# Performance work log

Hardware: AMD Instinct MI355X
Metric: run time of the kernel (lower is better)

## Reference

```python
import jax, jax.numpy as jnp
import numpy as np

B, N, DIM, HEADS = 8, 512, 512, 16
MAX_DIST, NG = 128, 32
RBF_STOP = 20.0
EPS = 1e-5


def _ln(x, g, b):
    m = jnp.mean(x, axis=-1, keepdims=True)
    v = jnp.mean((x - m) ** 2, axis=-1, keepdims=True)
    return (x - m) * jax.lax.rsqrt(v + EPS) * g + b


def setup_inputs() -> dict:
    key = jax.random.key(0)
    ks = jax.random.split(key, 12)
    d = DIM
    s = 0.02
    return {
        "x": jax.random.normal(ks[0], (B * N, d), jnp.float32),
        "dist_matrix": jax.random.randint(ks[1], (B, N, N), 0, MAX_DIST, jnp.int32),
        "dist_3d": jax.random.uniform(ks[2], (B, N, N), jnp.float32) * RBF_STOP,
        "norm1_g": jnp.ones((d,), jnp.float32),
        "norm1_b": jnp.zeros((d,), jnp.float32),
        "in_proj_w": jax.random.normal(ks[3], (3 * d, d), jnp.float32) * s,
        "in_proj_b": jnp.zeros((3 * d,), jnp.float32),
        "out_proj_w": jax.random.normal(ks[4], (d, d), jnp.float32) * s,
        "out_proj_b": jnp.zeros((d,), jnp.float32),
        "dist_emb": jax.random.normal(ks[5], (MAX_DIST, HEADS), jnp.float32) * s,
        "rbf_w": jax.random.normal(ks[6], (HEADS, NG), jnp.float32) * s,
        "rbf_b": jnp.zeros((HEADS,), jnp.float32),
        "norm2_g": jnp.ones((d,), jnp.float32),
        "norm2_b": jnp.zeros((d,), jnp.float32),
        "ffn_w1": jax.random.normal(ks[7], (4 * d, d), jnp.float32) * s,
        "ffn_b1": jnp.zeros((4 * d,), jnp.float32),
        "ffn_w2": jax.random.normal(ks[8], (d, 4 * d), jnp.float32) * s,
        "ffn_b2": jnp.zeros((d,), jnp.float32),
        "batch": jnp.repeat(jnp.arange(B, dtype=jnp.int32), N),
    }


def reference(x, dist_matrix, dist_3d, norm1_g, norm1_b, in_proj_w, in_proj_b,
              out_proj_w, out_proj_b, dist_emb, rbf_w, rbf_b, norm2_g, norm2_b,
              ffn_w1, ffn_b1, ffn_w2, ffn_b2, batch):
    b, n = dist_matrix.shape[0], dist_matrix.shape[1]
    d = x.shape[-1]
    dh = d // HEADS
    # equal-size graphs -> to_dense_batch is a reshape, mask all-true
    xd = x.reshape(b, n, d)

    # additive attention bias: shortest-path-distance embedding + RBF projection
    dc = jnp.clip(dist_matrix, 0, MAX_DIST - 1)
    bias_spd = dist_emb[dc]                                  # [b, n, n, H]
    offset = jnp.linspace(0.0, RBF_STOP, NG, dtype=jnp.float32)
    coeff = -0.5 / (RBF_STOP / (NG - 1)) ** 2
    rbf = jnp.exp(coeff * (dist_3d[..., None] - offset) ** 2)  # [b, n, n, NG]
    bias_3d = rbf @ rbf_w.T + rbf_b                          # [b, n, n, H]
    bias = jnp.transpose(bias_spd + bias_3d, (0, 3, 1, 2))   # [b, H, n, n]

    # multi-head attention (pre-norm residual, as in source)
    h = _ln(xd, norm1_g, norm1_b)
    qkv = h @ in_proj_w.T + in_proj_b
    q, k, v = jnp.split(qkv, 3, axis=-1)
    q = q.reshape(b, n, HEADS, dh).transpose(0, 2, 1, 3)
    k = k.reshape(b, n, HEADS, dh).transpose(0, 2, 1, 3)
    v = v.reshape(b, n, HEADS, dh).transpose(0, 2, 1, 3)
    scores = jnp.einsum('bhqd,bhkd->bhqk', q, k) / jnp.sqrt(jnp.float32(dh)) + bias
    attn = jax.nn.softmax(scores, axis=-1)
    ctx = jnp.einsum('bhqk,bhkd->bhqd', attn, v)
    ctx = ctx.transpose(0, 2, 1, 3).reshape(b, n, d)
    attn_out = ctx @ out_proj_w.T + out_proj_b
    h = h + attn_out

    # FFN (dropout inactive at eval)
    h2 = _ln(h, norm2_g, norm2_b)
    ff = jax.nn.gelu(h2 @ ffn_w1.T + ffn_b1, approximate=False) @ ffn_w2.T + ffn_b2
    h = h + ff
    return h.reshape(b * n, d)
```

## Files before the change

kernel.cpp:

```cpp
#include <hip/hip_runtime.h>
#include <hip/hip_bf16.h>
#include <math.h>

#define BB 8
#define NN 512
#define DD 512
#define NH 16
#define DH 32
#define TD 1536
#define NG 32
#define MAXD 128

typedef __attribute__((ext_vector_type(8))) short bf16x8;
typedef __attribute__((ext_vector_type(4))) float f32x4;
typedef __attribute__((ext_vector_type(2))) unsigned int u32x2;
typedef __attribute__((ext_vector_type(4))) unsigned int u32x4;

__device__ inline short f2bf(float x) {
    __hip_bfloat16 h = __float2bfloat16(x);
    return *reinterpret_cast<short*>(&h);
}
__device__ inline float bf2f(short x) {
    union { unsigned u; float f; } c;
    c.u = ((unsigned)(unsigned short)x) << 16;
    return c.f;
}
__device__ inline unsigned cvt_pk_bf16(float lo, float hi) {
    unsigned r;
    asm("v_cvt_pk_bf16_f32 %0, %1, %2" : "=v"(r) : "v"(lo), "v"(hi));
    return r;
}
__device__ inline float exp2fast(float x) {
    float r;
    asm("v_exp_f32 %0, %1" : "=v"(r) : "v"(x));
    return r;
}

__device__ inline void gld_lds16(const void* g, void* l) {
    __builtin_amdgcn_global_load_lds(
        (const __attribute__((address_space(1))) unsigned int*)g,
        (__attribute__((address_space(3))) unsigned int*)l, 16, 0, 0);
}

__global__ __launch_bounds__(256) void prep(
    const float* __restrict__ x, const float* __restrict__ n1g,
    const float* __restrict__ n1b, short* __restrict__ h_bf,
    const float* __restrict__ s0, const float* __restrict__ s1,
    const float* __restrict__ s2, const float* __restrict__ s3,
    short* __restrict__ d0, short* __restrict__ d1,
    short* __restrict__ d2, short* __restrict__ d3,
    const float* __restrict__ rbfw, const float* __restrict__ rbfb,
    short* __restrict__ Tg,
    int n0, int n1, int n2, int n3) {
    const int tid = threadIdx.x;
    if (blockIdx.x < 4096) {
        const int row = blockIdx.x;
        const int wave = tid >> 6, lane = tid & 63;
        const float* xr = x + (size_t)row * DD;
        const float2 v01 = *(const float2*)(xr + 2 * tid);
        float s = v01.x + v01.y, q = v01.x * v01.x + v01.y * v01.y;
#pragma unroll
        for (int m = 1; m < 64; m <<= 1) { s += __shfl_xor(s, m); q += __shfl_xor(q, m); }
        __shared__ float ps[8];
        if (lane == 0) { ps[wave] = s; ps[wave + 4] = q; }
        __syncthreads();
        s = ps[0] + ps[1] + ps[2] + ps[3];
        q = ps[4] + ps[5] + ps[6] + ps[7];
        const float mean = s * (1.0f / DD);
        const float var  = q * (1.0f / DD) - mean * mean;
        const float rs   = rsqrtf(var + 1e-5f);
        const float2 g2 = *(const float2*)(n1g + 2 * tid);
        const float2 b2 = *(const float2*)(n1b + 2 * tid);
        const float o0 = (v01.x - mean) * rs * g2.x + b2.x;
        const float o1 = (v01.y - mean) * rs * g2.y + b2.y;
        *(unsigned*)&h_bf[(size_t)row * DD + 2 * tid] = cvt_pk_bf16(o0, o1);
        return;
    }
    const int bx = blockIdx.x - 4096;
    const int y = bx >> 9, xb = bx & 511;
    if (y == 4) {
        if (xb != 0) return;
        const float STEP  = 20.0f / 31.0f;
        const float COEFF = -0.5f / (STEP * STEP);
        for (int idx = tid; idx < 194 * 16; idx += 256) {
            const int i = idx >> 4, h = idx & 15;
            const float xx = fminf((float)i, 192.0f) * (20.0f / 192.0f);
            float acc = rbfb[h];
#pragma unroll
            for (int g = 0; g < NG; g++) {
                const float t = xx - (float)g * STEP;
                acc += __expf(COEFF * t * t) * rbfw[h * NG + g];
            }
            Tg[idx] = f2bf(acc * 1.44269504088896f);
        }
        return;
    }
    const float* s; short* d; int n;
    switch (y) {
        case 0: s = s0; d = d0; n = n0; break;
        case 1: s = s1; d = d1; n = n1; break;
        case 2: s = s2; d = d2; n = n2; break;
        default: s = s3; d = d3; n = n3; break;
    }
    const int i = (xb * 256 + tid) * 8;
    if (i >= n) return;
    const float4 a = *(const float4*)(s + i);
    const float4 b = *(const float4*)(s + i + 4);
    u32x4 o;
    o[0] = cvt_pk_bf16(a.x, a.y);
    o[1] = cvt_pk_bf16(a.z, a.w);
    o[2] = cvt_pk_bf16(b.x, b.y);
    o[3] = cvt_pk_bf16(b.z, b.w);
    *(u32x4*)(d + i) = o;
}

template <int TM, bool GELU, int RESMODE, bool OUTBF>
__global__ __launch_bounds__(256) void gemm_bf16(
    const short* __restrict__ A, const short* __restrict__ Bw,
    const float* __restrict__ bias, const void* __restrict__ res,
    void* __restrict__ Cout, int M, int Nout, int K) {
    const int MI = (TM >= 32) ? TM / 32 : 1;
    const int bm = blockIdx.y * TM;
    const int bn = blockIdx.x * 128;
    const int tid  = threadIdx.x;
    const int wave = tid >> 6;
    const int lane = tid & 63;
    const int l16  = lane & 15;
    const int quad = lane >> 4;
    const int wr = (wave >> 1) * (TM / 2);
    const int wc = (wave & 1) * 64;

    __shared__ short As[2][TM * 32];
    __shared__ short Bs[2][128 * 32];

    f32x4 acc[MI][4];
#pragma unroll
    for (int i = 0; i < MI; i++)
#pragma unroll
        for (int j = 0; j < 4; j++) acc[i][j] = (f32x4){0.f, 0.f, 0.f, 0.f};

    auto stage = [&](int buf, int k0) {
        const short* Ab = A + (size_t)bm * K + k0;
        const short* Bb = Bw + (size_t)bn * K + k0;
        if (TM >= 64) {
#pragma unroll
            for (int j = 0; j < TM / 64; j++) {
                const int idx = j * 256 + tid;
                gld_lds16(Ab + (size_t)(idx >> 2) * K + (idx & 3) * 8,
                          &As[buf][(size_t)(j * 256 + wave * 64) * 8]);
            }
        } else {
            if (tid < 128)
                gld_lds16(Ab + (size_t)(tid >> 2) * K + (tid & 3) * 8,
                          &As[buf][(size_t)(wave * 64) * 8]);
        }
#pragma unroll
        for (int j = 0; j < 2; j++) {
            const int idx = j * 256 + tid;
            gld_lds16(Bb + (size_t)(idx >> 2) * K + (idx & 3) * 8,
                      &Bs[buf][(size_t)(j * 256 + wave * 64) * 8]);
        }
    };
    auto compute = [&](int buf) {
        bf16x8 af[MI], bfr[4];
#pragma unroll
        for (int i = 0; i < MI; i++)
            af[i] = *(const bf16x8*)&As[buf][(wr + i * 16 + l16) * 32 + quad * 8];
#pragma unroll
        for (int j = 0; j < 4; j++)
            bfr[j] = *(const bf16x8*)&Bs[buf][(wc + j * 16 + l16) * 32 + quad * 8];
#pragma unroll
        for (int i = 0; i < MI; i++)
#pragma unroll
            for (int j = 0; j < 4; j++)
                acc[i][j] = __builtin_amdgcn_mfma_f32_16x16x32_bf16(bfr[j], af[i], acc[i][j], 0, 0, 0);
    };

    stage(0, 0);
    __syncthreads();
    int cur = 0;
    for (int k0 = 32; k0 < K; k0 += 32) {
        stage(cur ^ 1, k0);
        compute(cur);
        __syncthreads();
        cur ^= 1;
    }
    compute(cur);

#pragma unroll
    for (int i = 0; i < MI; i++) {
        const int row = bm + wr + i * 16 + l16;
#pragma unroll
        for (int j = 0; j < 4; j++) {
            const int col = bn + wc + j * 16 + quad * 4;
            const float4 b4 = *(const float4*)&bias[col];
            float v[4] = {acc[i][j][0] + b4.x, acc[i][j][1] + b4.y,
                          acc[i][j][2] + b4.z, acc[i][j][3] + b4.w};
            if (GELU) {
#pragma unroll
                for (int r = 0; r < 4; r++)
                    v[r] = 0.5f * v[r] * (1.0f + erff(v[r] * 0.70710678118654752f));
            }
            if (RESMODE == 1) {
                const float4 r4 = *(const float4*)&((const float*)res)[(size_t)row * Nout + col];
                v[0] += r4.x; v[1] += r4.y; v[2] += r4.z; v[3] += r4.w;
            }
            if (RESMODE == 2) {
                const short4 r4 = *(const short4*)&((const short*)res)[(size_t)row * Nout + col];
                v[0] += bf2f(r4.x); v[1] += bf2f(r4.y); v[2] += bf2f(r4.z); v[3] += bf2f(r4.w);
            }
            if (OUTBF) {
                u32x2 o;
                o[0] = cvt_pk_bf16(v[0], v[1]);
                o[1] = cvt_pk_bf16(v[2], v[3]);
                *(u32x2*)&((short*)Cout)[(size_t)row * Nout + col] = o;
            } else {
                *(float4*)&((float*)Cout)[(size_t)row * Nout + col] =
                    (float4){v[0], v[1], v[2], v[3]};
            }
        }
    }
}

__global__ __launch_bounds__(512, 4) void attn_fused(
    const short* __restrict__ qkv,
    const int* __restrict__ dist,
    const float* __restrict__ dist3d,
    const float* __restrict__ demb,
    const short* __restrict__ Tg,
    const short* __restrict__ wo,
    const float* __restrict__ bo,
    const short* __restrict__ hb,
    const float* __restrict__ g2v,
    const float* __restrict__ b2v,
    float* __restrict__ hres,
    short* __restrict__ h2) {
    const int blk  = blockIdx.x;
    const int b    = blk & 7;
    const int q0   = (blk >> 3) * 16;
    const int tid  = threadIdx.x;
    const int wave = tid >> 6;
    const int lane = tid & 63;
    const int l16  = lane & 15;
    const int quad = lane >> 4;
    const int hh0  = wave * 2;

    __shared__ short Vc[NH * 1024];
    __shared__ short Pb[16 * 512];
    __shared__ short Tt[194 * 18];
    __shared__ short Db[128 * 18];
    __shared__ unsigned short Pk[512 * 16];
    __shared__ float St[2][16][8];

    for (int i = tid; i < 194 * 16; i += 512) Tt[(i >> 4) * 18 + (i & 15)] = Tg[i];
    for (int i = tid; i < 128 * 16; i += 512)
        Db[(i >> 4) * 18 + (i & 15)] = f2bf(demb[i] * 1.44269504088896f);
    {
        const size_t rb = ((size_t)(b * NN) + q0) * NN;
#pragma unroll
        for (int q = 0; q < 16; q++) {
            const size_t off = rb + (size_t)q * NN + tid;
            int dc = dist[off];
            dc = min(max(dc, 0), MAXD - 1);
            int ii = (int)(dist3d[off] * 9.6f + 0.5f);
            ii = min(ii, 192);
            Pk[tid * 16 + q] = (unsigned short)(dc | (ii << 8));
        }
    }

    const float scale = 0.17677669529663687f * 1.44269504088896f;
    bf16x8 qf[2];
#pragma unroll
    for (int h = 0; h < 2; h++)
        qf[h] = *(const bf16x8*)(qkv + (size_t)(b * NN + q0 + l16) * TD + (hh0 + h) * DH + quad * 8);

    f32x4 O[2][2];
    float lsum[2][4];
#pragma unroll
    for (int h = 0; h < 2; h++) {
#pragma unroll
        for (int tt = 0; tt < 2; tt++) O[h][tt] = (f32x4){0.f, 0.f, 0.f, 0.f};
#pragma unroll
        for (int r = 0; r < 4; r++) lsum[h][r] = 0.f;
    }

    __syncthreads();

    const int sk = lane >> 2;
    const int sc = lane & 3;

    auto stageV = [&](int c) {
        const size_t rowb = (size_t)(b * NN + c * 32 + sk) * TD + 2 * DD + sc * 8;
#pragma unroll
        for (int h = 0; h < 2; h++) {
            short* dst = &Vc[(hh0 + h) * 1024];
            gld_lds16(qkv + rowb + (hh0 + h) * DH, dst);
            gld_lds16(qkv + rowb + (size_t)16 * TD + (hh0 + h) * DH, dst + 512);
        }
    };
    auto loadK = [&](int c, bf16x8 (*kd)[2]) {
#pragma unroll
        for (int h = 0; h < 2; h++) {
            const short* base =
                qkv + (size_t)(b * NN + c * 32 + l16) * TD + DD + (hh0 + h) * DH + quad * 8;
            kd[h][0] = *(const bf16x8*)base;
            kd[h][1] = *(const bf16x8*)(base + 16 * TD);
        }
    };

    bf16x8 kf[2][2], kfn[2][2];
    stageV(0);
    loadK(0, kf);

    for (int c = 0; c < 16; c++) {
        asm volatile("" ::: "memory");
        __builtin_amdgcn_s_waitcnt(0x0F70);
        asm volatile("" ::: "memory");

        u32x2 vraw[2][4];
#pragma unroll
        for (int h = 0; h < 2; h++) {
            const unsigned va =
                (unsigned)(uintptr_t)&Vc[(hh0 + h) * 1024 + quad * 128 + l16];
            asm volatile("ds_read_b64_tr_b16 %0, %1 offset:0"    : "=v"(vraw[h][0]) : "v"(va));
            asm volatile("ds_read_b64_tr_b16 %0, %1 offset:128"  : "=v"(vraw[h][1]) : "v"(va));
            asm volatile("ds_read_b64_tr_b16 %0, %1 offset:1024" : "=v"(vraw[h][2]) : "v"(va));
            asm volatile("ds_read_b64_tr_b16 %0, %1 offset:1152" : "=v"(vraw[h][3]) : "v"(va));
        }
        asm volatile("s_waitcnt lgkmcnt(0)" ::: "memory");
        __builtin_amdgcn_sched_barrier(0);

        if (c + 1 < 16) {
            stageV(c + 1);
            loadK(c + 1, kfn);
        }

#pragma unroll
        for (int half = 0; half < 2; half++) {
            const ushort4 pk4 =
                *(const ushort4*)&Pk[(unsigned)((c * 32 + half * 16 + l16) * 16 + quad * 4)];
            const unsigned short pe[4] = {pk4.x, pk4.y, pk4.z, pk4.w};
            float bb[2][4];
#pragma unroll
            for (int r = 0; r < 4; r++) {
                const unsigned u  = pe[r];
                const unsigned dc = u & 0xFFu;
                const unsigned ii = u >> 8;
                const unsigned du = *(const unsigned*)&Db[dc * 18 + hh0];
                const unsigned tu = *(const unsigned*)&Tt[ii * 18 + hh0];
                union { unsigned x; float f; } a0, a1, b0, b1;
                a0.x = du << 16; a1.x = du & 0xFFFF0000u;
                b0.x = tu << 16; b1.x = tu & 0xFFFF0000u;
                bb[0][r] = a0.f + b0.f;
                bb[1][r] = a1.f + b1.f;
            }
#pragma unroll
            for (int h = 0; h < 2; h++) {
                f32x4 s = __builtin_amdgcn_mfma_f32_16x16x32_bf16(
                    qf[h], kf[h][half], (f32x4){0.f, 0.f, 0.f, 0.f}, 0, 0, 0);
                float pv[4];
#pragma unroll
                for (int r = 0; r < 4; r++) {
                    float sv = s[r] * scale + bb[h][r];
                    sv = fminf(sv, 28.853901f);
                    pv[r] = exp2fast(sv);
                    lsum[h][r] += pv[r];
                }
                u32x2 w;
                w[0] = cvt_pk_bf16(pv[0], pv[1]);
                w[1] = cvt_pk_bf16(pv[2], pv[3]);
                *(u32x2*)&Pb[(wave * 2 + h) * 512 + (half * 16 + l16) * 16 + quad * 4] = w;
            }
        }

        asm volatile("" ::: "memory");
        asm volatile("s_waitcnt lgkmcnt(0)" ::: "memory");
        __builtin_amdgcn_sched_barrier(0);

        u32x2 praw[2][2];
#pragma unroll
        for (int h = 0; h < 2; h++) {
            const unsigned pa =
                (unsigned)(uintptr_t)&Pb[(wave * 2 + h) * 512 + quad * 64 + l16];
            asm volatile("ds_read_b64_tr_b16 %0, %1 offset:0"   : "=v"(praw[h][0]) : "v"(pa));
            asm volatile("ds_read_b64_tr_b16 %0, %1 offset:512" : "=v"(praw[h][1]) : "v"(pa));
        }
        asm volatile("s_waitcnt lgkmcnt(0)" ::: "memory");
        __builtin_amdgcn_sched_barrier(0);

        __builtin_amdgcn_s_setprio(1);
#pragma unroll
        for (int h = 0; h < 2; h++) {
            union { u32x4 u; bf16x8 s; } pf, v0, v1;
            pf.u = (u32x4){praw[h][0][0], praw[h][0][1], praw[h][1][0], praw[h][1][1]};
#pragma unroll
            for (int r = 0; r < 4; r++) {
                v0.u[r] = __builtin_amdgcn_perm(vraw[h][r][1], vraw[h][r][0], 0x05040100u);
                v1.u[r] = __builtin_amdgcn_perm(vraw[h][r][1], vraw[h][r][0], 0x07060302u);
            }
            O[h][0] = __builtin_amdgcn_mfma_f32_16x16x32_bf16(pf.s, v0.s, O[h][0], 0, 0, 0);
            O[h][1] = __builtin_amdgcn_mfma_f32_16x16x32_bf16(pf.s, v1.s, O[h][1], 0, 0, 0);
        }
        __builtin_amdgcn_s_setprio(0);

#pragma unroll
        for (int h = 0; h < 2; h++) { kf[h][0] = kfn[h][0]; kf[h][1] = kfn[h][1]; }
    }

#pragma unroll
    for (int h = 0; h < 2; h++) {
#pragma unroll
        for (int m = 1; m < 16; m <<= 1)
#pragma unroll
            for (int r = 0; r < 4; r++) lsum[h][r] += __shfl_xor(lsum[h][r], m);
        float rl[4];
#pragma unroll
        for (int r = 0; r < 4; r++) rl[r] = 1.0f / lsum[h][r];
#pragma unroll
        for (int tt = 0; tt < 2; tt++) {
            const int col = (hh0 + h) * DH + tt * 16 + l16;
            u32x2 w;
            w[0] = cvt_pk_bf16(O[h][tt][0] * rl[0], O[h][tt][1] * rl[1]);
            w[1] = cvt_pk_bf16(O[h][tt][2] * rl[2], O[h][tt][3] * rl[3]);
            *(u32x2*)&Pb[col * 16 + quad * 4] = w;
        }
    }
    __syncthreads();

    const int rowg = b * NN + q0;
    const int wcol = wave * 64;
    short hbr[4][4];
#pragma unroll
    for (int j = 0; j < 4; j++)
#pragma unroll
        for (int r = 0; r < 4; r++)
            hbr[j][r] = hb[((size_t)rowg + quad * 4 + r) * DD + wcol + j * 16 + l16];

    f32x4 a2[4];
#pragma unroll
    for (int j = 0; j < 4; j++) a2[j] = (f32x4){0.f, 0.f, 0.f, 0.f};
    u32x2 blo[2][4], bhi[2][4];
#pragma unroll
    for (int j = 0; j < 4; j++) {
        const short* wb = wo + (size_t)(wcol + j * 16 + l16) * DD + quad * 4;
        blo[0][j] = *(const u32x2*)wb;
        bhi[0][j] = *(const u32x2*)(wb + 16);
    }
#pragma unroll
    for (int kk = 0; kk < 16; kk++) {
        const int k0 = kk * 32;
        u32x2 p0, p1;
        const unsigned pa = (unsigned)(uintptr_t)&Pb[k0 * 16 + quad * 64 + l16];
        asm volatile("ds_read_b64_tr_b16 %0, %1 offset:0"   : "=v"(p0) : "v"(pa));
        asm volatile("ds_read_b64_tr_b16 %0, %1 offset:512" : "=v"(p1) : "v"(pa));
        if (kk + 1 < 16) {
#pragma unroll
            for (int j = 0; j < 4; j++) {
                const short* wb =
                    wo + (size_t)(wcol + j * 16 + l16) * DD + (k0 + 32) + quad * 4;
                blo[(kk + 1) & 1][j] = *(const u32x2*)wb;
                bhi[(kk + 1) & 1][j] = *(const u32x2*)(wb + 16);
            }
        }
        asm volatile("s_waitcnt lgkmcnt(0)" ::: "memory");
        __builtin_amdgcn_sched_barrier(0);
        union { u32x4 u; bf16x8 s; } af;
        af.u = (u32x4){p0[0], p0[1], p1[0], p1[1]};
#pragma unroll
        for (int j = 0; j < 4; j++) {
            union { u32x4 u; bf16x8 s; } bw;
            bw.u = (u32x4){blo[kk & 1][j][0], blo[kk & 1][j][1],
                           bhi[kk & 1][j][0], bhi[kk & 1][j][1]};
            a2[j] = __builtin_amdgcn_mfma_f32_16x16x32_bf16(af.s, bw.s, a2[j], 0, 0, 0);
        }
    }

    float vv[4][4];
    float sp[4] = {0.f, 0.f, 0.f, 0.f}, qp[4] = {0.f, 0.f, 0.f, 0.f};
#pragma unroll
    for (int j = 0; j < 4; j++) {
        const int col = wcol + j * 16 + l16;
        const float bc = bo[col];
#pragma unroll
        for (int r = 0; r < 4; r++) {
            const size_t row = (size_t)rowg + quad * 4 + r;
            const float v = a2[j][r] + bc + bf2f(hbr[j][r]);
            hres[row * DD + col] = v;
            vv[j][r] = v;
            sp[r] += v; qp[r] += v * v;
        }
    }
#pragma unroll
    for (int m = 1; m < 16; m <<= 1)
#pragma unroll
        for (int r = 0; r < 4; r++) {
            sp[r] += __shfl_xor(sp[r], m);
            qp[r] += __shfl_xor(qp[r], m);
        }
    if (l16 == 0) {
#pragma unroll
        for (int r = 0; r < 4; r++) {
            St[0][quad * 4 + r][wave] = sp[r];
            St[1][quad * 4 + r][wave] = qp[r];
        }
    }
    __syncthreads();
    float mean[4], rsd[4];
#pragma unroll
    for (int r = 0; r < 4; r++) {
        const int rr = quad * 4 + r;
        float s = 0.f, q = 0.f;
#pragma unroll
        for (int w = 0; w < 8; w++) { s += St[0][rr][w]; q += St[1][rr][w]; }
        mean[r] = s * (1.0f / DD);
        rsd[r]  = rsqrtf(q * (1.0f / DD) - mean[r] * mean[r] + 1e-5f);
    }
#pragma unroll
    for (int j = 0; j < 4; j++) {
        const int col = wcol + j * 16 + l16;
        const float gc = g2v[col], bc2 = b2v[col];
#pragma unroll
        for (int r = 0; r < 4; r++) {
            const size_t row = (size_t)rowg + quad * 4 + r;
            h2[row * DD + col] = f2bf((vv[j][r] - mean[r]) * rsd[r] * gc + bc2);
        }
    }
}

extern "C" void kernel_launch(void* const* d_in, const int* in_sizes, int n_in,
                              void* d_out, int out_size, void* d_ws, size_t ws_size,
                              hipStream_t stream) {
    const float* x      = (const float*)d_in[0];
    const int*   dist   = (const int*)d_in[1];
    const float* dist3d = (const float*)d_in[2];
    const float* n1g    = (const float*)d_in[3];
    const float* n1b    = (const float*)d_in[4];
    const float* win    = (const float*)d_in[5];
    const float* bin    = (const float*)d_in[6];
    const float* wo     = (const float*)d_in[7];
    const float* bo     = (const float*)d_in[8];
    const float* demb   = (const float*)d_in[9];
    const float* rbfw   = (const float*)d_in[10];
    const float* rbfb   = (const float*)d_in[11];
    const float* n2g    = (const float*)d_in[12];
    const float* n2b    = (const float*)d_in[13];
    const float* w1     = (const float*)d_in[14];
    const float* b1     = (const float*)d_in[15];
    const float* w2     = (const float*)d_in[16];
    const float* b2     = (const float*)d_in[17];

    char* p = (char*)d_ws;
    short* h_bf   = (short*)p; p += (size_t)4096 * 512 * 2;
    short* qkv_bf = (short*)p; p += (size_t)4096 * 1536 * 2;
    float* hres   = (float*)p; p += (size_t)4096 * 512 * 4;
    short* h2_bf  = (short*)p; p += (size_t)4096 * 512 * 2;
    short* win_bf = (short*)p; p += (size_t)1536 * 512 * 2;
    short* wo_bf  = (short*)p; p += (size_t)512 * 512 * 2;
    short* w1_bf  = (short*)p; p += (size_t)2048 * 512 * 2;
    short* w2_bf  = (short*)p; p += (size_t)512 * 2048 * 2;
    short* Tg     = (short*)p; p += (size_t)8192;
    short* mid_bf = (short*)p; p += (size_t)4096 * 2048 * 2;

    const int M = BB * NN;

    prep<<<4096 + 2560, 256, 0, stream>>>(
        x, n1g, n1b, h_bf,
        win, wo, w1, w2, win_bf, wo_bf, w1_bf, w2_bf, rbfw, rbfb, Tg,
        1536 * 512, 512 * 512, 2048 * 512, 512 * 2048);
    gemm_bf16<128, false, 0, true><<<dim3(12, 32), 256, 0, stream>>>(
        h_bf, win_bf, bin, nullptr, qkv_bf, M, TD, DD);
    attn_fused<<<256, 512, 0, stream>>>(
        qkv_bf, dist, dist3d, demb, Tg, wo_bf, bo, h_bf, n2g, n2b, hres, h2_bf);
    gemm_bf16<128, true, 0, true><<<dim3(16, 32), 256, 0, stream>>>(
        h2_bf, w1_bf, b1, nullptr, mid_bf, M, 2048, DD);
    gemm_bf16<32, false, 1, false><<<dim3(4, 128), 256, 0, stream>>>(
        mid_bf, w2_bf, b2, hres, (float*)d_out, M, DD, 2048);
}
```

Baseline: 260.2 us.

## Use one wave per head in fused attention with 1024-thread blocks

The fused attention kernel goes from 8 waves each handling two heads to 16 waves each handling one head, doubling the block size to 1024 threads. The out-projection/LayerNorm epilogue is re-split so each wave owns 32 output columns instead of 64, and the row statistics reduce over 16 waves. The aim is more latency hiding and less per-wave serial work, since the grid has only 256 blocks. In exchange the bias lookup now does separate 16-bit loads per head, and 1024-thread blocks limit how many blocks fit per CU and raise per-block sync cost.

```diff
diff --git a/kernel.cpp b/kernel.cpp
--- a/kernel.cpp
+++ b/kernel.cpp
@@ -222,7 +222,7 @@
     }
 }
 
-__global__ __launch_bounds__(512, 4) void attn_fused(
+__global__ __launch_bounds__(1024, 4) void attn_fused(
     const short* __restrict__ qkv,
     const int* __restrict__ dist,
     const float* __restrict__ dist3d,
@@ -243,46 +243,41 @@
     const int lane = tid & 63;
     const int l16  = lane & 15;
     const int quad = lane >> 4;
-    const int hh0  = wave * 2;
+    const int hh   = wave;
 
     __shared__ short Vc[NH * 1024];
     __shared__ short Pb[16 * 512];
     __shared__ short Tt[194 * 18];
     __shared__ short Db[128 * 18];
     __shared__ unsigned short Pk[512 * 16];
-    __shared__ float St[2][16][8];
-
-    for (int i = tid; i < 194 * 16; i += 512) Tt[(i >> 4) * 18 + (i & 15)] = Tg[i];
-    for (int i = tid; i < 128 * 16; i += 512)
+    __shared__ float St[2][16][16];
+
+    for (int i = tid; i < 194 * 16; i += 1024) Tt[(i >> 4) * 18 + (i & 15)] = Tg[i];
+    for (int i = tid; i < 128 * 16; i += 1024)
         Db[(i >> 4) * 18 + (i & 15)] = f2bf(demb[i] * 1.44269504088896f);
     {
         const size_t rb = ((size_t)(b * NN) + q0) * NN;
-#pragma unroll
-        for (int q = 0; q < 16; q++) {
-            const size_t off = rb + (size_t)q * NN + tid;
+        for (int i = tid; i < 16 * 512; i += 1024) {
+            const int q = i >> 9, k = i & 511;
+            const size_t off = rb + (size_t)q * NN + k;
             int dc = dist[off];
             dc = min(max(dc, 0), MAXD - 1);
             int ii = (int)(dist3d[off] * 9.6f + 0.5f);
             ii = min(ii, 192);
-            Pk[tid * 16 + q] = (unsigned short)(dc | (ii << 8));
+            Pk[k * 16 + q] = (unsigned short)(dc | (ii << 8));
         }
     }
 
     const float scale = 0.17677669529663687f * 1.44269504088896f;
-    bf16x8 qf[2];
-#pragma unroll
-    for (int h = 0; h < 2; h++)
-        qf[h] = *(const bf16x8*)(qkv + (size_t)(b * NN + q0 + l16) * TD + (hh0 + h) * DH + quad * 8);
-
-    f32x4 O[2][2];
-    float lsum[2][4];
-#pragma unroll
-    for (int h = 0; h < 2; h++) {
-#pragma unroll
-        for (int tt = 0; tt < 2; tt++) O[h][tt] = (f32x4){0.f, 0.f, 0.f, 0.f};
-#pragma unroll
-        for (int r = 0; r < 4; r++) lsum[h][r] = 0.f;
-    }
+    const bf16x8 qf =
+        *(const bf16x8*)(qkv + (size_t)(b * NN + q0 + l16) * TD + hh * DH + quad * 8);
+
+    f32x4 O[2];
+    float lsum[4];
+#pragma unroll
+    for (int tt = 0; tt < 2; tt++) O[tt] = (f32x4){0.f, 0.f, 0.f, 0.f};
+#pragma unroll
+    for (int r = 0; r < 4; r++) lsum[r] = 0.f;
 
     __syncthreads();
 
@@ -291,24 +286,18 @@
 
     auto stageV = [&](int c) {
         const size_t rowb = (size_t)(b * NN + c * 32 + sk) * TD + 2 * DD + sc * 8;
-#pragma unroll
-        for (int h = 0; h < 2; h++) {
-            short* dst = &Vc[(hh0 + h) * 1024];
-            gld_lds16(qkv + rowb + (hh0 + h) * DH, dst);
-            gld_lds16(qkv + rowb + (size_t)16 * TD + (hh0 + h) * DH, dst + 512);
-        }
+        short* dst = &Vc[hh * 1024];
+        gld_lds16(qkv + rowb + hh * DH, dst);
+        gld_lds16(qkv + rowb + (size_t)16 * TD + hh * DH, dst + 512);
     };
-    auto loadK = [&](int c, bf16x8 (*kd)[2]) {
-#pragma unroll
-        for (int h = 0; h < 2; h++) {
-            const short* base =
-                qkv + (size_t)(b * NN + c * 32 + l16) * TD + DD + (hh0 + h) * DH + quad * 8;
-            kd[h][0] = *(const bf16x8*)base;
-            kd[h][1] = *(const bf16x8*)(base + 16 * TD);
-        }
+    auto loadK = [&](int c, bf16x8* kd) {
+        const short* base =
+            qkv + (size_t)(b * NN + c * 32 + l16) * TD + DD + hh * DH + quad * 8;
+        kd[0] = *(const bf16x8*)base;
+        kd[1] = *(const bf16x8*)(base + 16 * TD);
     };
 
-    bf16x8 kf[2][2], kfn[2][2];
+    bf16x8 kf[2], kfn[2];
     stageV(0);
     loadK(0, kf);
 
@@ -317,15 +306,14 @@
         __builtin_amdgcn_s_waitcnt(0x0F70);
         asm volatile("" ::: "memory");
 
-        u32x2 vraw[2][4];
-#pragma unroll
-        for (int h = 0; h < 2; h++) {
+        u32x2 vraw[4];
+        {
             const unsigned va =
-                (unsigned)(uintptr_t)&Vc[(hh0 + h) * 1024 + quad * 128 + l16];
-            asm volatile("ds_read_b64_tr_b16 %0, %1 offset:0"    : "=v"(vraw[h][0]) : "v"(va));
-            asm volatile("ds_read_b64_tr_b16 %0, %1 offset:128"  : "=v"(vraw[h][1]) : "v"(va));
-            asm volatile("ds_read_b64_tr_b16 %0, %1 offset:1024" : "=v"(vraw[h][2]) : "v"(va));
-            asm volatile("ds_read_b64_tr_b16 %0, %1 offset:1152" : "=v"(vraw[h][3]) : "v"(va));
+                (unsigned)(uintptr_t)&Vc[hh * 1024 + quad * 128 + l16];
+            asm volatile("ds_read_b64_tr_b16 %0, %1 offset:0"    : "=v"(vraw[0]) : "v"(va));
+            asm volatile("ds_read_b64_tr_b16 %0, %1 offset:128"  : "=v"(vraw[1]) : "v"(va));
+            asm volatile("ds_read_b64_tr_b16 %0, %1 offset:1024" : "=v"(vraw[2]) : "v"(va));
+            asm volatile("ds_read_b64_tr_b16 %0, %1 offset:1152" : "=v"(vraw[3]) : "v"(va));
         }
         asm volatile("s_waitcnt lgkmcnt(0)" ::: "memory");
         __builtin_amdgcn_sched_barrier(0);
@@ -340,108 +328,93 @@
             const ushort4 pk4 =
                 *(const ushort4*)&Pk[(unsigned)((c * 32 + half * 16 + l16) * 16 + quad * 4)];
             const unsigned short pe[4] = {pk4.x, pk4.y, pk4.z, pk4.w};
-            float bb[2][4];
+            float bb[4];
 #pragma unroll
             for (int r = 0; r < 4; r++) {
                 const unsigned u  = pe[r];
                 const unsigned dc = u & 0xFFu;
                 const unsigned ii = u >> 8;
-                const unsigned du = *(const unsigned*)&Db[dc * 18 + hh0];
-                const unsigned tu = *(const unsigned*)&Tt[ii * 18 + hh0];
-                union { unsigned x; float f; } a0, a1, b0, b1;
-                a0.x = du << 16; a1.x = du & 0xFFFF0000u;
-                b0.x = tu << 16; b1.x = tu & 0xFFFF0000u;
-                bb[0][r] = a0.f + b0.f;
-                bb[1][r] = a1.f + b1.f;
-            }
-#pragma unroll
-            for (int h = 0; h < 2; h++) {
-                f32x4 s = __builtin_amdgcn_mfma_f32_16x16x32_bf16(
-                    qf[h], kf[h][half], (f32x4){0.f, 0.f, 0.f, 0.f}, 0, 0, 0);
-                float pv[4];
-#pragma unroll
-                for (int r = 0; r < 4; r++) {
-                    float sv = s[r] * scale + bb[h][r];
-                    sv = fminf(sv, 28.853901f);
-                    pv[r] = exp2fast(sv);
-                    lsum[h][r] += pv[r];
-                }
-                u32x2 w;
-                w[0] = cvt_pk_bf16(pv[0], pv[1]);
-                w[1] = cvt_pk_bf16(pv[2], pv[3]);
-                *(u32x2*)&Pb[(wave * 2 + h) * 512 + (half * 16 + l16) * 16 + quad * 4] = w;
-            }
+                bb[r] = bf2f(Db[dc * 18 + hh]) + bf2f(Tt[ii * 18 + hh]);
+            }
+            f32x4 s = __builtin_amdgcn_mfma_f32_16x16x32_bf16(
+                qf, kf[half], (f32x4){0.f, 0.f, 0.f, 0.f}, 0, 0, 0);
+            float pv[4];
+#pragma unroll
+            for (int r = 0; r < 4; r++) {
+                float sv = s[r] * scale + bb[r];
+                sv = fminf(sv, 28.853901f);
+                pv[r] = exp2fast(sv);
+                lsum[r] += pv[r];
+            }
+            u32x2 w;
+            w[0] = cvt_pk_bf16(pv[0], pv[1]);
+            w[1] = cvt_pk_bf16(pv[2], pv[3]);
+            *(u32x2*)&Pb[wave * 512 + (half * 16 + l16) * 16 + quad * 4] = w;
         }
 
         asm volatile("" ::: "memory");
         asm volatile("s_waitcnt lgkmcnt(0)" ::: "memory");
         __builtin_amdgcn_sched_barrier(0);
 
-        u32x2 praw[2][2];
-#pragma unroll
-        for (int h = 0; h < 2; h++) {
+        u32x2 praw[2];
+        {
             const unsigned pa =
-                (unsigned)(uintptr_t)&Pb[(wave * 2 + h) * 512 + quad * 64 + l16];
-            asm volatile("ds_read_b64_tr_b16 %0, %1 offset:0"   : "=v"(praw[h][0]) : "v"(pa));
-            asm volatile("ds_read_b64_tr_b16 %0, %1 offset:512" : "=v"(praw[h][1]) : "v"(pa));
+                (unsigned)(uintptr_t)&Pb[wave * 512 + quad * 64 + l16];
+            asm volatile("ds_read_b64_tr_b16 %0, %1 offset:0"   : "=v"(praw[0]) : "v"(pa));
+            asm volatile("ds_read_b64_tr_b16 %0, %1 offset:512" : "=v"(praw[1]) : "v"(pa));
         }
         asm volatile("s_waitcnt lgkmcnt(0)" ::: "memory");
         __builtin_amdgcn_sched_barrier(0);
 
         __builtin_amdgcn_s_setprio(1);
-#pragma unroll
-        for (int h = 0; h < 2; h++) {
+        {
             union { u32x4 u; bf16x8 s; } pf, v0, v1;
-            pf.u = (u32x4){praw[h][0][0], praw[h][0][1], praw[h][1][0], praw[h][1][1]};
+            pf.u = (u32x4){praw[0][0], praw[0][1], praw[1][0], praw[1][1]};
 #pragma unroll
             for (int r = 0; r < 4; r++) {
-                v0.u[r] = __builtin_amdgcn_perm(vraw[h][r][1], vraw[h][r][0], 0x05040100u);
-                v1.u[r] = __builtin_amdgcn_perm(vraw[h][r][1], vraw[h][r][0], 0x07060302u);
-            }
-            O[h][0] = __builtin_amdgcn_mfma_f32_16x16x32_bf16(pf.s, v0.s, O[h][0], 0, 0, 0);
-            O[h][1] = __builtin_amdgcn_mfma_f32_16x16x32_bf16(pf.s, v1.s, O[h][1], 0, 0, 0);
+                v0.u[r] = __builtin_amdgcn_perm(vraw[r][1], vraw[r][0], 0x05040100u);
+                v1.u[r] = __builtin_amdgcn_perm(vraw[r][1], vraw[r][0], 0x07060302u);
+            }
+            O[0] = __builtin_amdgcn_mfma_f32_16x16x32_bf16(pf.s, v0.s, O[0], 0, 0, 0);
+            O[1] = __builtin_amdgcn_mfma_f32_16x16x32_bf16(pf.s, v1.s, O[1], 0, 0, 0);
         }
         __builtin_amdgcn_s_setprio(0);
 
-#pragma unroll
-        for (int h = 0; h < 2; h++) { kf[h][0] = kfn[h][0]; kf[h][1] = kfn[h][1]; }
-    }
-
-#pragma unroll
-    for (int h = 0; h < 2; h++) {
-#pragma unroll
-        for (int m = 1; m < 16; m <<= 1)
-#pragma unroll
-            for (int r = 0; r < 4; r++) lsum[h][r] += __shfl_xor(lsum[h][r], m);
-        float rl[4];
-#pragma unroll
-        for (int r = 0; r < 4; r++) rl[r] = 1.0f / lsum[h][r];
-#pragma unroll
-        for (int tt = 0; tt < 2; tt++) {
-            const int col = (hh0 + h) * DH + tt * 16 + l16;
-            u32x2 w;
-            w[0] = cvt_pk_bf16(O[h][tt][0] * rl[0], O[h][tt][1] * rl[1]);
-            w[1] = cvt_pk_bf16(O[h][tt][2] * rl[2], O[h][tt][3] * rl[3]);
-            *(u32x2*)&Pb[col * 16 + quad * 4] = w;
-        }
+        kf[0] = kfn[0]; kf[1] = kfn[1];
+    }
+
+#pragma unroll
+    for (int m = 1; m < 16; m <<= 1)
+#pragma unroll
+        for (int r = 0; r < 4; r++) lsum[r] += __shfl_xor(lsum[r], m);
+    float rl[4];
+#pragma unroll
+    for (int r = 0; r < 4; r++) rl[r] = 1.0f / lsum[r];
+#pragma unroll
+    for (int tt = 0; tt < 2; tt++) {
+        const int col = hh * DH + tt * 16 + l16;
+        u32x2 w;
+        w[0] = cvt_pk_bf16(O[tt][0] * rl[0], O[tt][1] * rl[1]);
+        w[1] = cvt_pk_bf16(O[tt][2] * rl[2], O[tt][3] * rl[3]);
+        *(u32x2*)&Pb[col * 16 + quad * 4] = w;
     }
     __syncthreads();
 
     const int rowg = b * NN + q0;
-    const int wcol = wave * 64;
-    short hbr[4][4];
-#pragma unroll
-    for (int j = 0; j < 4; j++)
+    const int wcol = wave * 32;
+    short hbr[2][4];
+#pragma unroll
+    for (int j = 0; j < 2; j++)
 #pragma unroll
         for (int r = 0; r < 4; r++)
             hbr[j][r] = hb[((size_t)rowg + quad * 4 + r) * DD + wcol + j * 16 + l16];
 
-    f32x4 a2[4];
-#pragma unroll
-    for (int j = 0; j < 4; j++) a2[j] = (f32x4){0.f, 0.f, 0.f, 0.f};
-    u32x2 blo[2][4], bhi[2][4];
-#pragma unroll
-    for (int j = 0; j < 4; j++) {
+    f32x4 a2[2];
+#pragma unroll
+    for (int j = 0; j < 2; j++) a2[j] = (f32x4){0.f, 0.f, 0.f, 0.f};
+    u32x2 blo[2][2], bhi[2][2];
+#pragma unroll
+    for (int j = 0; j < 2; j++) {
         const short* wb = wo + (size_t)(wcol + j * 16 + l16) * DD + quad * 4;
         blo[0][j] = *(const u32x2*)wb;
         bhi[0][j] = *(const u32x2*)(wb + 16);
@@ -455,7 +428,7 @@
         asm volatile("ds_read_b64_tr_b16 %0, %1 offset:512" : "=v"(p1) : "v"(pa));
         if (kk + 1 < 16) {
 #pragma unroll
-            for (int j = 0; j < 4; j++) {
+            for (int j = 0; j < 2; j++) {
                 const short* wb =
                     wo + (size_t)(wcol + j * 16 + l16) * DD + (k0 + 32) + quad * 4;
                 blo[(kk + 1) & 1][j] = *(const u32x2*)wb;
@@ -467,7 +440,7 @@
         union { u32x4 u; bf16x8 s; } af;
         af.u = (u32x4){p0[0], p0[1], p1[0], p1[1]};
 #pragma unroll
-        for (int j = 0; j < 4; j++) {
+        for (int j = 0; j < 2; j++) {
             union { u32x4 u; bf16x8 s; } bw;
             bw.u = (u32x4){blo[kk & 1][j][0], blo[kk & 1][j][1],
                            bhi[kk & 1][j][0], bhi[kk & 1][j][1]};
@@ -475,10 +448,10 @@
         }
     }
 
-    float vv[4][4];
+    float vv[2][4];
     float sp[4] = {0.f, 0.f, 0.f, 0.f}, qp[4] = {0.f, 0.f, 0.f, 0.f};
 #pragma unroll
-    for (int j = 0; j < 4; j++) {
+    for (int j = 0; j < 2; j++) {
         const int col = wcol + j * 16 + l16;
         const float bc = bo[col];
 #pragma unroll
@@ -511,12 +484,12 @@
         const int rr = quad * 4 + r;
         float s = 0.f, q = 0.f;
 #pragma unroll
-        for (int w = 0; w < 8; w++) { s += St[0][rr][w]; q += St[1][rr][w]; }
+        for (int w = 0; w < 16; w++) { s += St[0][rr][w]; q += St[1][rr][w]; }
         mean[r] = s * (1.0f / DD);
         rsd[r]  = rsqrtf(q * (1.0f / DD) - mean[r] * mean[r] + 1e-5f);
     }
 #pragma unroll
-    for (int j = 0; j < 4; j++) {
+    for (int j = 0; j < 2; j++) {
         const int col = wcol + j * 16 + l16;
         const float gc = g2v[col], bc2 = b2v[col];
 #pragma unroll
@@ -569,7 +542,7 @@
         1536 * 512, 512 * 512, 2048 * 512, 512 * 2048);
     gemm_bf16<128, false, 0, true><<<dim3(12, 32), 256, 0, stream>>>(
         h_bf, win_bf, bin, nullptr, qkv_bf, M, TD, DD);
-    attn_fused<<<256, 512, 0, stream>>>(
+    attn_fused<<<256, 1024, 0, stream>>>(
         qkv_bf, dist, dist3d, demb, Tg, wo_bf, bo, h_bf, n2g, n2b, hres, h2_bf);
     gemm_bf16<128, true, 0, true><<<dim3(16, 32), 256, 0, stream>>>(
         h2_bf, w1_bf, b1, nullptr, mid_bf, M, 2048, DD);
```

Result: no change. 263.8 us (+1.4%).
